# Kernel optimization log

Hardware: AMD Instinct MI355X
Metric: run time of the kernel (lower is better)

The kernel has to match this reference:

```python
import jax, jax.numpy as jnp
import numpy as np

HIDDEN = 32
INPUT = 1


def setup_inputs() -> dict:
    key = jax.random.key(0)
    ks = jax.random.split(key, 8)
    B, T = 4096, 512
    s = 1.0 / np.sqrt(HIDDEN)
    return {
        "x": jax.random.normal(ks[0], (B, T, INPUT), dtype=jnp.float32),
        "h0": jnp.zeros((1, B, HIDDEN), dtype=jnp.float32),
        "W_ih": jax.random.uniform(ks[1], (HIDDEN, INPUT), jnp.float32, -s, s),
        "b_ih": jax.random.uniform(ks[2], (HIDDEN,), jnp.float32, -s, s),
        "W_hh": jax.random.uniform(ks[3], (HIDDEN, HIDDEN), jnp.float32, -s, s),
        "b_hh": jax.random.uniform(ks[4], (HIDDEN,), jnp.float32, -s, s),
        "W_out": jax.random.uniform(ks[5], (1, HIDDEN), jnp.float32, -s, s),
        "b_out": jax.random.uniform(ks[6], (1,), jnp.float32, -s, s),
    }


def reference(x, h0, W_ih, b_ih, W_hh, b_hh, W_out, b_out):
    # Precompute input projection for all timesteps: [B, T, H]
    xp = jnp.einsum("bti,hi->bth", x, W_ih) + b_ih

    def step(h, xt):  # h: [B,H], xt: [B,H]
        h_new = jnp.tanh(xt + h @ W_hh.T + b_hh)
        return h_new, h_new

    hT, r_out = jax.lax.scan(step, h0[0], jnp.swapaxes(xp, 0, 1))  # r_out: [T,B,H]
    r_out = jnp.swapaxes(r_out, 0, 1)  # [B,T,H]
    # Per-timestep Linear(32->1) fused into one batched matmul
    outs = jnp.einsum("bth,oh->bto", r_out, W_out) + b_out  # [B,T,1]
    return outs, hT[None]  # h_state: [1,B,H]
```

## Files before the change

### kernel.cpp

```cpp
#include <hip/hip_runtime.h>

#define BATCH 4096
#define SEQT  512
#define HID   32
#define CH    32
#define ROWP  40
#define WPB   4

typedef _Float16 f16;
typedef _Float16 h2 __attribute__((ext_vector_type(2)));

#if __has_builtin(__builtin_amdgcn_fdot2)
#define FDOT2(a, b, c) __builtin_amdgcn_fdot2((a), (b), (c), false)
#else
#define FDOT2(a, b, c) fmaf((float)(a)[1], (float)(b)[1], fmaf((float)(a)[0], (float)(b)[0], (c)))
#endif

#if __has_builtin(__builtin_amdgcn_exp2f)
#define FAST_EXP2(x) __builtin_amdgcn_exp2f(x)
#else
#define FAST_EXP2(x) exp2f(x)
#endif
#if __has_builtin(__builtin_amdgcn_rcpf)
#define FAST_RCP(x) __builtin_amdgcn_rcpf(x)
#else
#define FAST_RCP(x) (1.0f / (x))
#endif

#define BC(x) __builtin_bit_cast(h2, (x))

__global__ __launch_bounds__(64 * WPB, 2) void rnn_kernel(
    const float* __restrict__ x,
    const float* __restrict__ h0,
    const float* __restrict__ W_ih,
    const float* __restrict__ b_ih,
    const float* __restrict__ W_hh,
    const float* __restrict__ b_hh,
    const float* __restrict__ W_out,
    const float* __restrict__ b_out,
    float* __restrict__ out)
{
    const int tid  = threadIdx.x;
    const int wv   = tid >> 6;
    const int lane = tid & 63;
    const int g    = lane >> 5;
    const int j    = lane & 31;
    const int bseq = blockIdx.x * (2 * WPB) + 2 * wv + g;

    __shared__ f16   hist_s[WPB][2][CH][ROWP];
    __shared__ float xbuf_s[WPB][2][CH];

    f16*   hist = &hist_s[wv][g][0][0];
    float* xbuf = &xbuf_s[wv][g][0];

    h2 Wr[16];
    {
        const float4* wrow = reinterpret_cast<const float4*>(W_hh + j * HID);
        #pragma unroll
        for (int m = 0; m < 8; ++m) {
            float4 v = wrow[m];
            Wr[2 * m + 0] = h2{(f16)v.x, (f16)v.y};
            Wr[2 * m + 1] = h2{(f16)v.z, (f16)v.w};
        }
    }
    h2 Wo[16];
    {
        const float4* wrow = reinterpret_cast<const float4*>(W_out);
        #pragma unroll
        for (int m = 0; m < 8; ++m) {
            float4 v = wrow[m];
            Wo[2 * m + 0] = h2{(f16)v.x, (f16)v.y};
            Wo[2 * m + 1] = h2{(f16)v.z, (f16)v.w};
        }
    }
    const float wih  = W_ih[j];
    const float bias = b_ih[j] + b_hh[j];
    const float bout = b_out[0];

    hist[(CH - 1) * ROWP + j] = (f16)h0[bseq * HID + j];
    __builtin_amdgcn_wave_barrier();

    const float* xg = x + (size_t)bseq * SEQT;
    float*       og = out + (size_t)bseq * SEQT;

    float hT = 0.0f;

    for (int tc = 0; tc < SEQT; tc += CH) {
        xbuf[j] = xg[tc + j];
        __builtin_amdgcn_wave_barrier();

        float xc = xbuf[0];

        #pragma unroll
        for (int t2 = 0; t2 < CH; ++t2) {
            const f16* rp = hist + ((t2 + CH - 1) & (CH - 1)) * ROWP;
            const float4 q0 = reinterpret_cast<const float4*>(rp)[0];
            const float4 q1 = reinterpret_cast<const float4*>(rp)[1];
            const float4 q2 = reinterpret_cast<const float4*>(rp)[2];
            const float4 q3 = reinterpret_cast<const float4*>(rp)[3];
            const float xn = xbuf[(t2 + 1) & (CH - 1)];

            float a0 = fmaf(xc, wih, bias);
            a0 = FDOT2(BC(q0.x), Wr[0],  a0);
            float a1 = FDOT2(BC(q0.y), Wr[1],  0.0f);
            float a2 = FDOT2(BC(q0.z), Wr[2],  0.0f);
            float a3 = FDOT2(BC(q0.w), Wr[3],  0.0f);
            a0 = FDOT2(BC(q1.x), Wr[4],  a0);
            a1 = FDOT2(BC(q1.y), Wr[5],  a1);
            a2 = FDOT2(BC(q1.z), Wr[6],  a2);
            a3 = FDOT2(BC(q1.w), Wr[7],  a3);
            a0 = FDOT2(BC(q2.x), Wr[8],  a0);
            a1 = FDOT2(BC(q2.y), Wr[9],  a1);
            a2 = FDOT2(BC(q2.z), Wr[10], a2);
            a3 = FDOT2(BC(q2.w), Wr[11], a3);
            a0 = FDOT2(BC(q3.x), Wr[12], a0);
            a1 = FDOT2(BC(q3.y), Wr[13], a1);
            a2 = FDOT2(BC(q3.z), Wr[14], a2);
            a3 = FDOT2(BC(q3.w), Wr[15], a3);
            const float part = (a0 + a1) + (a2 + a3);

            const float e  = FAST_EXP2(part * 2.8853900817779268f);
            const float hn = fmaf(-2.0f, FAST_RCP(e + 1.0f), 1.0f);

            hist[t2 * ROWP + j] = (f16)hn;
            __builtin_amdgcn_wave_barrier();

            xc = xn;
            hT = hn;
        }

        {
            const f16* rp = hist + j * ROWP;
            const float4 q0 = reinterpret_cast<const float4*>(rp)[0];
            const float4 q1 = reinterpret_cast<const float4*>(rp)[1];
            const float4 q2 = reinterpret_cast<const float4*>(rp)[2];
            const float4 q3 = reinterpret_cast<const float4*>(rp)[3];
            float o0 = FDOT2(BC(q0.x), Wo[0],  bout);
            float o1 = FDOT2(BC(q0.y), Wo[1],  0.0f);
            float o2 = FDOT2(BC(q0.z), Wo[2],  0.0f);
            float o3 = FDOT2(BC(q0.w), Wo[3],  0.0f);
            o0 = FDOT2(BC(q1.x), Wo[4],  o0);
            o1 = FDOT2(BC(q1.y), Wo[5],  o1);
            o2 = FDOT2(BC(q1.z), Wo[6],  o2);
            o3 = FDOT2(BC(q1.w), Wo[7],  o3);
            o0 = FDOT2(BC(q2.x), Wo[8],  o0);
            o1 = FDOT2(BC(q2.y), Wo[9],  o1);
            o2 = FDOT2(BC(q2.z), Wo[10], o2);
            o3 = FDOT2(BC(q2.w), Wo[11], o3);
            o0 = FDOT2(BC(q3.x), Wo[12], o0);
            o1 = FDOT2(BC(q3.y), Wo[13], o1);
            o2 = FDOT2(BC(q3.z), Wo[14], o2);
            o3 = FDOT2(BC(q3.w), Wo[15], o3);
            og[tc + j] = (o0 + o1) + (o2 + o3);
        }
        __builtin_amdgcn_wave_barrier();
    }

    out[(size_t)BATCH * SEQT + (size_t)bseq * HID + j] = hT;
}

extern "C" void kernel_launch(void* const* d_in, const int* in_sizes, int n_in,
                              void* d_out, int out_size, void* d_ws, size_t ws_size,
                              hipStream_t stream) {
    const float* x     = (const float*)d_in[0];
    const float* h0    = (const float*)d_in[1];
    const float* W_ih  = (const float*)d_in[2];
    const float* b_ih  = (const float*)d_in[3];
    const float* W_hh  = (const float*)d_in[4];
    const float* b_hh  = (const float*)d_in[5];
    const float* W_out = (const float*)d_in[6];
    const float* b_out = (const float*)d_in[7];
    float* outp = (float*)d_out;

    dim3 grid(BATCH / (2 * WPB));
    dim3 block(64 * WPB);
    hipLaunchKernelGGL(rnn_kernel, grid, block, 0, stream,
                       x, h0, W_ih, b_ih, W_hh, b_hh, W_out, b_out, outp);
}
```

Measured before the change: 158.8 us.

## Keep hidden state in registers and exchange it across lanes with DPP instead of LDS

Each sequence now uses 16 lanes, and each lane owns two hidden units. The hidden state stays in registers and is broadcast across lanes with DPP xor-permutes, while W_hh columns are pre-permuted to match, so the per-step LDS store, barrier and reload go away. The output projection is computed every step with a DPP butterfly reduction, and x is prefetched from global memory in double-buffered float4 chunks. The trade-off is more permute instructions per step and twice the FMA work per lane, in exchange for four sequences per wave and no shared-memory latency on the recurrence's critical path.

```diff
diff --git a/kernel.cpp b/kernel.cpp
--- a/kernel.cpp
+++ b/kernel.cpp
@@ -3,9 +3,6 @@
 #define BATCH 4096
 #define SEQT  512
 #define HID   32
-#define CH    32
-#define ROWP  40
-#define WPB   4
 
 typedef _Float16 f16;
 typedef _Float16 h2 __attribute__((ext_vector_type(2)));
@@ -27,9 +24,26 @@
 #define FAST_RCP(x) (1.0f / (x))
 #endif
 
-#define BC(x) __builtin_bit_cast(h2, (x))
+#define DPP_X1  0xB1
+#define DPP_X2  0x4E
+#define DPP_X7  0x141
+#define DPP_X15 0x140
 
-__global__ __launch_bounds__(64 * WPB, 2) void rnn_kernel(
+#if __has_builtin(__builtin_amdgcn_update_dpp)
+template <int C, typename T>
+__device__ __forceinline__ T xl(T v) {
+    return __builtin_bit_cast(T, __builtin_amdgcn_update_dpp(
+        0, __builtin_bit_cast(int, v), C, 0xF, 0xF, false));
+}
+#else
+template <int C, typename T>
+__device__ __forceinline__ T xl(T v) {
+    constexpr int m = (C == DPP_X1) ? 1 : (C == DPP_X2) ? 2 : (C == DPP_X7) ? 7 : 15;
+    return __builtin_bit_cast(T, __shfl_xor(__builtin_bit_cast(int, v), m));
+}
+#endif
+
+__global__ __launch_bounds__(256) void rnn_kernel(
     const float* __restrict__ x,
     const float* __restrict__ h0,
     const float* __restrict__ W_ih,
@@ -41,122 +55,118 @@
     float* __restrict__ out)
 {
     const int tid  = threadIdx.x;
-    const int wv   = tid >> 6;
-    const int lane = tid & 63;
-    const int g    = lane >> 5;
-    const int j    = lane & 31;
-    const int bseq = blockIdx.x * (2 * WPB) + 2 * wv + g;
+    const int ell  = tid & 15;
+    const int bseq = (blockIdx.x * 256 + tid) >> 4;
+    const int j0 = 2 * ell, j1 = 2 * ell + 1;
 
-    __shared__ f16   hist_s[WPB][2][CH][ROWP];
-    __shared__ float xbuf_s[WPB][2][CH];
+    constexpr int MTBL[16] = {0, 1, 2, 3, 7, 6, 5, 4, 15, 14, 13, 12, 8, 9, 10, 11};
 
-    f16*   hist = &hist_s[wv][g][0][0];
-    float* xbuf = &xbuf_s[wv][g][0];
-
-    h2 Wr[16];
-    {
-        const float4* wrow = reinterpret_cast<const float4*>(W_hh + j * HID);
-        #pragma unroll
-        for (int m = 0; m < 8; ++m) {
-            float4 v = wrow[m];
-            Wr[2 * m + 0] = h2{(f16)v.x, (f16)v.y};
-            Wr[2 * m + 1] = h2{(f16)v.z, (f16)v.w};
-        }
+    h2 W0[16], W1[16];
+    #pragma unroll
+    for (int r = 0; r < 16; ++r) {
+        const int p = ell ^ MTBL[r];
+        const float2 w0 = *reinterpret_cast<const float2*>(W_hh + j0 * HID + 2 * p);
+        const float2 w1 = *reinterpret_cast<const float2*>(W_hh + j1 * HID + 2 * p);
+        W0[r] = h2{(f16)w0.x, (f16)w0.y};
+        W1[r] = h2{(f16)w1.x, (f16)w1.y};
     }
-    h2 Wo[16];
-    {
-        const float4* wrow = reinterpret_cast<const float4*>(W_out);
-        #pragma unroll
-        for (int m = 0; m < 8; ++m) {
-            float4 v = wrow[m];
-            Wo[2 * m + 0] = h2{(f16)v.x, (f16)v.y};
-            Wo[2 * m + 1] = h2{(f16)v.z, (f16)v.w};
-        }
-    }
-    const float wih  = W_ih[j];
-    const float bias = b_ih[j] + b_hh[j];
+    const float2 wo = *reinterpret_cast<const float2*>(W_out + j0);
+    const h2 Wo2 = h2{(f16)wo.x, (f16)wo.y};
+    const float wih0 = W_ih[j0], wih1 = W_ih[j1];
+    const float bia0 = b_ih[j0] + b_hh[j0];
+    const float bia1 = b_ih[j1] + b_hh[j1];
     const float bout = b_out[0];
 
-    hist[(CH - 1) * ROWP + j] = (f16)h0[bseq * HID + j];
-    __builtin_amdgcn_wave_barrier();
+    const float2 h0v = *reinterpret_cast<const float2*>(h0 + (size_t)bseq * HID + j0);
+    h2 hcur = h2{(f16)h0v.x, (f16)h0v.y};
+    float hn0 = h0v.x, hn1 = h0v.y;
 
     const float* xg = x + (size_t)bseq * SEQT;
     float*       og = out + (size_t)bseq * SEQT;
 
-    float hT = 0.0f;
+#define STEP(T2, XC) do {                                                     \
+    h2 v0 = hcur;                                                             \
+    h2 v1 = xl<DPP_X1>(v0);                                                   \
+    h2 v2 = xl<DPP_X2>(v0);                                                   \
+    h2 v3 = xl<DPP_X2>(v1);                                                   \
+    h2 v4 = xl<DPP_X7>(v0);                                                   \
+    h2 v5 = xl<DPP_X7>(v1);                                                   \
+    h2 v6 = xl<DPP_X7>(v2);                                                   \
+    h2 v7 = xl<DPP_X7>(v3);                                                   \
+    h2 v8  = xl<DPP_X15>(v0);                                                 \
+    h2 v9  = xl<DPP_X15>(v1);                                                 \
+    h2 v10 = xl<DPP_X15>(v2);                                                 \
+    h2 v11 = xl<DPP_X15>(v3);                                                 \
+    h2 v12 = xl<DPP_X15>(v4);                                                 \
+    h2 v13 = xl<DPP_X15>(v5);                                                 \
+    h2 v14 = xl<DPP_X15>(v6);                                                 \
+    h2 v15 = xl<DPP_X15>(v7);                                                 \
+    float a0 = fmaf((XC), wih0, bia0);                                        \
+    float b0 = fmaf((XC), wih1, bia1);                                        \
+    a0 = FDOT2(v0,  W0[0],  a0);                                              \
+    float a1 = FDOT2(v1,  W0[1],  0.0f);                                      \
+    float a2 = FDOT2(v2,  W0[2],  0.0f);                                      \
+    float a3 = FDOT2(v3,  W0[3],  0.0f);                                      \
+    a0 = FDOT2(v4,  W0[4],  a0); a1 = FDOT2(v5,  W0[5],  a1);                 \
+    a2 = FDOT2(v6,  W0[6],  a2); a3 = FDOT2(v7,  W0[7],  a3);                 \
+    a0 = FDOT2(v8,  W0[8],  a0); a1 = FDOT2(v9,  W0[9],  a1);                 \
+    a2 = FDOT2(v10, W0[10], a2); a3 = FDOT2(v11, W0[11], a3);                 \
+    a0 = FDOT2(v12, W0[12], a0); a1 = FDOT2(v13, W0[13], a1);                 \
+    a2 = FDOT2(v14, W0[14], a2); a3 = FDOT2(v15, W0[15], a3);                 \
+    b0 = FDOT2(v0,  W1[0],  b0);                                              \
+    float b1 = FDOT2(v1,  W1[1],  0.0f);                                      \
+    float b2 = FDOT2(v2,  W1[2],  0.0f);                                      \
+    float b3 = FDOT2(v3,  W1[3],  0.0f);                                      \
+    b0 = FDOT2(v4,  W1[4],  b0); b1 = FDOT2(v5,  W1[5],  b1);                 \
+    b2 = FDOT2(v6,  W1[6],  b2); b3 = FDOT2(v7,  W1[7],  b3);                 \
+    b0 = FDOT2(v8,  W1[8],  b0); b1 = FDOT2(v9,  W1[9],  b1);                 \
+    b2 = FDOT2(v10, W1[10], b2); b3 = FDOT2(v11, W1[11], b3);                 \
+    b0 = FDOT2(v12, W1[12], b0); b1 = FDOT2(v13, W1[13], b1);                 \
+    b2 = FDOT2(v14, W1[14], b2); b3 = FDOT2(v15, W1[15], b3);                 \
+    const float s0 = (a0 + a1) + (a2 + a3);                                   \
+    const float s1 = (b0 + b1) + (b2 + b3);                                   \
+    const float e0 = FAST_EXP2(s0 * 2.8853900817779268f);                     \
+    const float e1 = FAST_EXP2(s1 * 2.8853900817779268f);                     \
+    hn0 = fmaf(-2.0f, FAST_RCP(e0 + 1.0f), 1.0f);                             \
+    hn1 = fmaf(-2.0f, FAST_RCP(e1 + 1.0f), 1.0f);                             \
+    hcur = h2{(f16)hn0, (f16)hn1};                                            \
+    float pp = FDOT2(hcur, Wo2, 0.0f);                                        \
+    pp += xl<DPP_X1>(pp);                                                     \
+    pp += xl<DPP_X2>(pp);                                                     \
+    pp += xl<DPP_X7>(pp);                                                     \
+    pp += xl<DPP_X15>(pp);                                                    \
+    if (ell == (T2)) osel = pp;                                               \
+} while (0)
 
-    for (int tc = 0; tc < SEQT; tc += CH) {
-        xbuf[j] = xg[tc + j];
-        __builtin_amdgcn_wave_barrier();
+#define HALF(HC, Q0, Q1, Q2, Q3) do {                                         \
+    float osel = 0.0f;                                                        \
+    STEP(0,  (Q0).x); STEP(1,  (Q0).y); STEP(2,  (Q0).z); STEP(3,  (Q0).w);   \
+    STEP(4,  (Q1).x); STEP(5,  (Q1).y); STEP(6,  (Q1).z); STEP(7,  (Q1).w);   \
+    STEP(8,  (Q2).x); STEP(9,  (Q2).y); STEP(10, (Q2).z); STEP(11, (Q2).w);   \
+    STEP(12, (Q3).x); STEP(13, (Q3).y); STEP(14, (Q3).z); STEP(15, (Q3).w);   \
+    og[(HC) * 16 + ell] = osel + bout;                                        \
+} while (0)
 
-        float xc = xbuf[0];
+    const float4* xq0 = reinterpret_cast<const float4*>(xg);
+    float4 qA0 = xq0[0], qA1 = xq0[1], qA2 = xq0[2], qA3 = xq0[3];
+    float4 qB0, qB1, qB2, qB3;
 
-        #pragma unroll
-        for (int t2 = 0; t2 < CH; ++t2) {
-            const f16* rp = hist + ((t2 + CH - 1) & (CH - 1)) * ROWP;
-            const float4 q0 = reinterpret_cast<const float4*>(rp)[0];
-            const float4 q1 = reinterpret_cast<const float4*>(rp)[1];
-            const float4 q2 = reinterpret_cast<const float4*>(rp)[2];
-            const float4 q3 = reinterpret_cast<const float4*>(rp)[3];
-            const float xn = xbuf[(t2 + 1) & (CH - 1)];
-
-            float a0 = fmaf(xc, wih, bias);
-            a0 = FDOT2(BC(q0.x), Wr[0],  a0);
-            float a1 = FDOT2(BC(q0.y), Wr[1],  0.0f);
-            float a2 = FDOT2(BC(q0.z), Wr[2],  0.0f);
-            float a3 = FDOT2(BC(q0.w), Wr[3],  0.0f);
-            a0 = FDOT2(BC(q1.x), Wr[4],  a0);
-            a1 = FDOT2(BC(q1.y), Wr[5],  a1);
-            a2 = FDOT2(BC(q1.z), Wr[6],  a2);
-            a3 = FDOT2(BC(q1.w), Wr[7],  a3);
-            a0 = FDOT2(BC(q2.x), Wr[8],  a0);
-            a1 = FDOT2(BC(q2.y), Wr[9],  a1);
-            a2 = FDOT2(BC(q2.z), Wr[10], a2);
-            a3 = FDOT2(BC(q2.w), Wr[11], a3);
-            a0 = FDOT2(BC(q3.x), Wr[12], a0);
-            a1 = FDOT2(BC(q3.y), Wr[13], a1);
-            a2 = FDOT2(BC(q3.z), Wr[14], a2);
-            a3 = FDOT2(BC(q3.w), Wr[15], a3);
-            const float part = (a0 + a1) + (a2 + a3);
-
-            const float e  = FAST_EXP2(part * 2.8853900817779268f);
-            const float hn = fmaf(-2.0f, FAST_RCP(e + 1.0f), 1.0f);
-
-            hist[t2 * ROWP + j] = (f16)hn;
-            __builtin_amdgcn_wave_barrier();
-
-            xc = xn;
-            hT = hn;
-        }
-
-        {
-            const f16* rp = hist + j * ROWP;
-            const float4 q0 = reinterpret_cast<const float4*>(rp)[0];
-            const float4 q1 = reinterpret_cast<const float4*>(rp)[1];
-            const float4 q2 = reinterpret_cast<const float4*>(rp)[2];
-            const float4 q3 = reinterpret_cast<const float4*>(rp)[3];
-            float o0 = FDOT2(BC(q0.x), Wo[0],  bout);
-            float o1 = FDOT2(BC(q0.y), Wo[1],  0.0f);
-            float o2 = FDOT2(BC(q0.z), Wo[2],  0.0f);
-            float o3 = FDOT2(BC(q0.w), Wo[3],  0.0f);
-            o0 = FDOT2(BC(q1.x), Wo[4],  o0);
-            o1 = FDOT2(BC(q1.y), Wo[5],  o1);
-            o2 = FDOT2(BC(q1.z), Wo[6],  o2);
-            o3 = FDOT2(BC(q1.w), Wo[7],  o3);
-            o0 = FDOT2(BC(q2.x), Wo[8],  o0);
-            o1 = FDOT2(BC(q2.y), Wo[9],  o1);
-            o2 = FDOT2(BC(q2.z), Wo[10], o2);
-            o3 = FDOT2(BC(q2.w), Wo[11], o3);
-            o0 = FDOT2(BC(q3.x), Wo[12], o0);
-            o1 = FDOT2(BC(q3.y), Wo[13], o1);
-            o2 = FDOT2(BC(q3.z), Wo[14], o2);
-            o3 = FDOT2(BC(q3.w), Wo[15], o3);
-            og[tc + j] = (o0 + o1) + (o2 + o3);
-        }
-        __builtin_amdgcn_wave_barrier();
+    #pragma unroll 1
+    for (int hc = 0; hc < 32; hc += 2) {
+        const float4* pB = reinterpret_cast<const float4*>(xg + (hc + 1) * 16);
+        qB0 = pB[0]; qB1 = pB[1]; qB2 = pB[2]; qB3 = pB[3];
+        HALF(hc, qA0, qA1, qA2, qA3);
+        const int tn = (hc + 2 < 32) ? (hc + 2) : 0;
+        const float4* pA = reinterpret_cast<const float4*>(xg + tn * 16);
+        qA0 = pA[0]; qA1 = pA[1]; qA2 = pA[2]; qA3 = pA[3];
+        HALF(hc + 1, qB0, qB1, qB2, qB3);
     }
 
-    out[(size_t)BATCH * SEQT + (size_t)bseq * HID + j] = hT;
+    float2 ht; ht.x = hn0; ht.y = hn1;
+    *reinterpret_cast<float2*>(out + (size_t)BATCH * SEQT + (size_t)bseq * HID + j0) = ht;
+
+#undef HALF
+#undef STEP
 }
 
 extern "C" void kernel_launch(void* const* d_in, const int* in_sizes, int n_in,
@@ -172,8 +182,8 @@
     const float* b_out = (const float*)d_in[7];
     float* outp = (float*)d_out;
 
-    dim3 grid(BATCH / (2 * WPB));
-    dim3 block(64 * WPB);
+    dim3 grid(BATCH * 16 / 256);
+    dim3 block(256);
     hipLaunchKernelGGL(rnn_kernel, grid, block, 0, stream,
                        x, h0, W_ih, b_ih, W_hh, b_hh, W_out, b_out, outp);
 }
```

Result: slower. 168.6 us (+6.2%).
